# Optimization experiments

Measured on AMD Instinct MI355X. Metric: run time of the kernel, lower is better.

The kernel has to match this reference:

```python
import jax, jax.numpy as jnp
import numpy as np

T = 2048        # document length in tokens
L = 10          # max span width (compute_idx_spans default)
ATTN_DIM = 1024 # states feature dim
EMBED_DIM = 1024
DIST_DIM = 20
HID = 150       # Score hidden_dim default
GI_DIM = 2 * ATTN_DIM + EMBED_DIM + DIST_DIM
BINS = np.array([1, 2, 3, 4, 8, 16, 32, 64])
NEG = -1e10


def _mlp(x, W1, b1, W2, b2, W3, b3):
    # Score module: Linear -> ReLU -> Linear -> ReLU -> Linear (dropout = eval identity)
    h = jax.nn.relu(x @ W1 + b1)
    h = jax.nn.relu(h @ W2 + b2)
    return h @ W3 + b3


def setup_inputs() -> dict:
    key = jax.random.key(0)
    ks = jax.random.split(key, 16)
    s = 0.02
    return {
        "states": jax.random.normal(ks[0], (T, ATTN_DIM), jnp.float32),
        "embeds": jax.random.normal(ks[1], (T, EMBED_DIM), jnp.float32),
        # attention Score (input ATTN_DIM)
        "attn_W1": s * jax.random.normal(ks[2], (ATTN_DIM, HID), jnp.float32),
        "attn_b1": jnp.zeros((HID,), jnp.float32),
        "attn_W2": s * jax.random.normal(ks[3], (HID, HID), jnp.float32),
        "attn_b2": jnp.zeros((HID,), jnp.float32),
        "attn_W3": s * jax.random.normal(ks[4], (HID, 1), jnp.float32),
        "attn_b3": jnp.zeros((1,), jnp.float32),
        # width distance embedding table (len(bins)+1 = 9 rows)
        "width_table": s * jax.random.normal(ks[5], (len(BINS) + 1, DIST_DIM), jnp.float32),
        # mention Score (input GI_DIM)
        "score_W1": s * jax.random.normal(ks[6], (GI_DIM, HID), jnp.float32),
        "score_b1": jnp.zeros((HID,), jnp.float32),
        "score_W2": s * jax.random.normal(ks[7], (HID, HID), jnp.float32),
        "score_b2": jnp.zeros((HID,), jnp.float32),
        "score_W3": s * jax.random.normal(ks[8], (HID, 1), jnp.float32),
        "score_b3": jnp.zeros((1,), jnp.float32),
    }


def reference(states, embeds,
              attn_W1, attn_b1, attn_W2, attn_b2, attn_W3, attn_b3,
              width_table,
              score_W1, score_b1, score_W2, score_b2, score_W3, score_b3):
    # Enumerate all spans with start in [0, T-L] and width 1..L (static shapes).
    starts = jnp.arange(T - L + 1)
    widths = jnp.arange(1, L + 1)
    i1 = jnp.repeat(starts, L)                 # [N]
    w = jnp.tile(widths, T - L + 1)            # [N]
    i2 = i1 + w - 1
    pos = i1[:, None] + jnp.arange(L)[None, :]  # [N, L] (max index T-1)
    mask = jnp.arange(L)[None, :] < w[:, None]  # [N, L]

    # Per-token attention scores, then ragged gather + masked softmax pooling.
    attns = _mlp(states, attn_W1, attn_b1, attn_W2, attn_b2, attn_W3, attn_b3)  # [T, 1]
    span_attns = jnp.where(mask, attns[pos, 0], NEG)        # [N, L] (pad value -1e10)
    attn_weights = jax.nn.softmax(span_attns, axis=1)        # [N, L]
    attn_embeds = jnp.einsum('nl,nle->ne', attn_weights, embeds[pos])  # [N, E]

    # Width bucket embedding: stoi = #bins <= length.
    bin_idx = jnp.searchsorted(jnp.asarray(BINS), w, side='right')
    width_emb = width_table[bin_idx]                         # [N, DIST_DIM]

    start_end = jnp.concatenate([states[i1], states[i2]], axis=1)  # [N, 2*ATTN_DIM]
    g_i = jnp.concatenate([start_end, attn_embeds, width_emb], axis=1)  # [N, GI_DIM]
    mention_scores = _mlp(g_i, score_W1, score_b1, score_W2, score_b2, score_W3, score_b3)  # [N, 1]
    return mention_scores
```

## Files before the change

kernel.cpp:

```cpp
#include <hip/hip_runtime.h>

#define T_TOK 2048
#define AD    1024
#define HID   150
#define LW    10
#define NSTART (T_TOK - LW + 1)
#define NSPAN  (NSTART * LW)
#define RS    152

#define OFF_AH  0
#define OFF_SA  (OFF_AH + T_TOK*RS)
#define OFF_SB  (OFF_SA + T_TOK*RS)
#define OFF_EC  (OFF_SB + T_TOK*RS)
#define OFF_WT  (OFF_EC + T_TOK*RS)
#define OFF_ATT (OFF_WT + 16*RS)
#define OFF_BF16 (OFF_ATT + T_TOK)

typedef __attribute__((ext_vector_type(8))) short bf16x8;
typedef __attribute__((ext_vector_type(4))) float f32x4;

__device__ inline unsigned short f2bf(float f) {
  unsigned u = __builtin_bit_cast(unsigned, f);
  u += 0x7fff + ((u >> 16) & 1);
  return (unsigned short)(u >> 16);
}

__device__ inline unsigned cvt2(float lo, float hi) {
  unsigned r;
  asm("v_cvt_pk_bf16_f32 %0, %1, %2" : "=v"(r) : "v"(lo), "v"(hi));
  return r;
}

__device__ inline void gld16(const void* g, void* l) {
  __builtin_amdgcn_global_load_lds(
      (const __attribute__((address_space(1))) unsigned int*)g,
      (__attribute__((address_space(3))) unsigned int*)l, 16, 0, 0);
}

__global__ __launch_bounds__(256) void k_pack(
    const float* __restrict__ aw1, const float* __restrict__ sw1,
    const float* __restrict__ sw2, const float* __restrict__ aw2,
    const float* __restrict__ width_table, const float* __restrict__ score_b1,
    unsigned short* __restrict__ Wt,
    unsigned short* __restrict__ W2t, unsigned short* __restrict__ AW2t,
    float* __restrict__ ws) {
  __shared__ unsigned short T[152*72];
  const int b = blockIdx.x, t = threadIdx.x;

  if (b < 64) {
    const int grp = b >> 4, kt = b & 15;
    const float* src = (grp == 0) ? aw1 : sw1 + (size_t)(grp-1)*AD*HID;
    const int k0 = kt * 64;
    for (int idx = t; idx < 64*152; idx += 256) {
      int kl = idx / 152, j = idx - kl*152;
      float v = (j < HID) ? src[(size_t)(k0+kl)*HID + j] : 0.f;
      T[j*72 + kl] = f2bf(v);
    }
    __syncthreads();
    for (int u = t; u < 160*8; u += 256) {
      int jj = u >> 3, kc = u & 7;
      bf16x8 v;
      if (jj < 152) v = *(const bf16x8*)&T[jj*72 + kc*8];
      else          v = (bf16x8){0,0,0,0,0,0,0,0};
      *(bf16x8*)&Wt[(size_t)(grp*160 + jj)*AD + k0 + kc*8] = v;
    }
  } else if (b < 264) {
    int idx = (b - 64) * 256 + t;
    const float* src; unsigned short* dst; int u;
    if (idx < 25600) { src = sw2; dst = W2t; u = idx; }
    else             { src = aw2; dst = AW2t; u = idx - 25600; }
    int j = u / 160, k = u - j*160;
    float v = (j < HID && k < HID) ? src[(size_t)k*HID + j] : 0.f;
    dst[u] = f2bf(v);
  } else {
    const int j = t;
    if (j < HID) {
      float* WT = ws + OFF_WT;
      for (int bb = 0; bb < 9; ++bb) {
        float acc = score_b1[j];
#pragma unroll
        for (int d = 0; d < 20; ++d)
          acc = fmaf(width_table[bb*20 + d], sw1[(size_t)(3*AD + d)*HID + j], acc);
        WT[bb*RS + j] = acc;
      }
    }
  }
}

#define BM 32
#define KS 64
__global__ __launch_bounds__(320) void k_gemm(
    const float* __restrict__ st, const float* __restrict__ em,
    const unsigned short* __restrict__ Wt, const float* __restrict__ attn_b1,
    float* __restrict__ ws) {
  const int m0   = blockIdx.x * BM;
  const int s    = blockIdx.y >> 1;
  const int half = blockIdx.y & 1;
  const int tid  = threadIdx.x;
  const int lane = tid & 63, wv = tid >> 6;

  __shared__ unsigned short lA[2][BM*KS];
  __shared__ unsigned short lB[2][80*KS];

  const float* Ag = (s < 3 ? st : em) + (size_t)m0 * AD;
  const unsigned short* Bg = Wt + (size_t)(s*160 + half*80) * AD;

  f32x4 acc0 = {0.f,0.f,0.f,0.f}, acc1 = {0.f,0.f,0.f,0.f};

  auto stageB = [&](int kb, int buf) {
    for (int seg = wv; seg < 10; seg += 5) {
      int c = seg*64 + lane;
      int row = c >> 3, ch = c & 7;
      gld16(Bg + (size_t)row*AD + kb + ((ch ^ (row & 7)) << 3), &lB[buf][seg*512]);
    }
  };
  auto stageA = [&](int kb, int buf) {
    if (tid < 256) {
      int row = tid >> 3, ch = tid & 7;
      const float* src = Ag + (size_t)row*AD + kb + ((ch ^ (row & 7)) << 3);
      float4 a = *(const float4*)src;
      float4 c = *(const float4*)(src + 4);
      uint4 o;
      o.x = cvt2(a.x, a.y); o.y = cvt2(a.z, a.w);
      o.z = cvt2(c.x, c.y); o.w = cvt2(c.z, c.w);
      *(uint4*)&lA[buf][tid*8] = o;
    }
  };

  stageB(0, 0);
  stageA(0, 0);
  int buf = 0;
  const int r = lane & 15, g = lane >> 4;
  const int rx = wv*16 + r;
  const int sw = r & 7;

  for (int kk = 0; kk < 16; ++kk) {
    __syncthreads();
    if (kk < 15) { stageB((kk+1)*KS, buf ^ 1); stageA((kk+1)*KS, buf ^ 1); }
#pragma unroll
    for (int z = 0; z < 2; ++z) {
      const int cz = z*4 + g;
      bf16x8 X  = *(const bf16x8*)&lB[buf][rx*KS      + ((cz ^ sw) << 3)];
      bf16x8 Y0 = *(const bf16x8*)&lA[buf][r*KS       + ((cz ^ sw) << 3)];
      bf16x8 Y1 = *(const bf16x8*)&lA[buf][(16+r)*KS  + ((cz ^ sw) << 3)];
      acc0 = __builtin_amdgcn_mfma_f32_16x16x32_bf16(X, Y0, acc0, 0, 0, 0);
      acc1 = __builtin_amdgcn_mfma_f32_16x16x32_bf16(X, Y1, acc1, 0, 0, 0);
    }
    buf ^= 1;
  }

  const int jn = half*80 + wv*16 + g*4;
  float* Cp = ws + (s==0 ? OFF_AH : s==1 ? OFF_SA : s==2 ? OFF_SB : OFF_EC);
#pragma unroll
  for (int f = 0; f < 2; ++f) {
    int m = m0 + f*16 + r;
    f32x4 a = f ? acc1 : acc0;
    if (s == 0) {
#pragma unroll
      for (int q = 0; q < 4; ++q)
        if (jn + q < HID) a[q] = fmaxf(a[q] + attn_b1[jn+q], 0.f);
    }
    float* d = Cp + (size_t)m*RS + jn;
    if (jn + 3 < HID) *(f32x4*)d = a;
    else {
#pragma unroll
      for (int q = 0; q < 4; ++q) if (jn + q < HID) d[q] = a[q];
    }
  }
}

#define PS 168

#define SPB 8
__global__ __launch_bounds__(640) void k_span(
    const unsigned short* __restrict__ W2t,
    const unsigned short* __restrict__ AW2t,
    const float* __restrict__ ab2, const float* __restrict__ aw3,
    const float* __restrict__ ab3,
    const float* __restrict__ sb2, const float* __restrict__ sw3,
    const float* __restrict__ sb3,
    const float* __restrict__ ws, float* __restrict__ out) {
  const int i1b = blockIdx.x * SPB;
  const int t = threadIdx.x, lane = t & 63, wv = t >> 6;
  const int r = lane & 15, g = lane >> 4;
  __shared__ unsigned short sH[80 * PS];
  __shared__ float red[80][10];
  __shared__ float sATT[32];
  __shared__ float sE[SPB][10], sI[SPB][10];
  const float* AH = ws + OFF_AH;

  for (int u = t; u < 32*160; u += 640) {
    int row = u / 160, jj = u - row*160;
    int tok = i1b + row;
    float v = (row < 17 && jj < HID && tok < T_TOK) ? AH[(size_t)tok*RS + jj] : 0.f;
    sH[row*PS + jj] = f2bf(v);
  }
  __syncthreads();
  {
    const int jt = wv;
    bf16x8 Af[5];
#pragma unroll
    for (int kc = 0; kc < 5; ++kc)
      Af[kc] = *(const bf16x8*)&AW2t[(size_t)(jt*16 + r)*160 + kc*32 + g*8];
    f32x4 acc[2];
#pragma unroll
    for (int nt = 0; nt < 2; ++nt) acc[nt] = (f32x4){0.f,0.f,0.f,0.f};
#pragma unroll
    for (int nt = 0; nt < 2; ++nt)
#pragma unroll
      for (int kc = 0; kc < 5; ++kc) {
        bf16x8 Bf = *(const bf16x8*)&sH[(nt*16 + r)*PS + kc*32 + g*8];
        acc[nt] = __builtin_amdgcn_mfma_f32_16x16x32_bf16(Af[kc], Bf, acc[nt], 0, 0, 0);
      }
    float b2v[4], w3v[4];
#pragma unroll
    for (int q = 0; q < 4; ++q) {
      int j = jt*16 + g*4 + q;
      b2v[q] = (j < HID) ? ab2[j] : 0.f;
      w3v[q] = (j < HID) ? aw3[j] : 0.f;
    }
#pragma unroll
    for (int nt = 0; nt < 2; ++nt) {
      float p = 0.f;
#pragma unroll
      for (int q = 0; q < 4; ++q)
        p += fmaxf(acc[nt][q] + b2v[q], 0.f) * w3v[q];
      p += __shfl_xor(p, 16);
      p += __shfl_xor(p, 32);
      if (g == 0) red[nt*16 + r][wv] = p;
    }
  }
  __syncthreads();
  if (t < 32) {
    float s = ab3[0];
#pragma unroll
    for (int w = 0; w < 10; ++w) s += red[t][w];
    sATT[t] = s;
  }
  __syncthreads();

  if (t < SPB) {
    int i1 = i1b + t;
    if (i1 < NSTART) {
      float a[10];
#pragma unroll
      for (int l = 0; l < 10; ++l) a[l] = sATT[t + l];
      float M = a[0];
#pragma unroll
      for (int l = 1; l < 10; ++l) M = fmaxf(M, a[l]);
      float D = 0.f;
#pragma unroll
      for (int l = 0; l < 10; ++l) {
        float e = expf(a[l] - M);
        D += e;
        sE[t][l] = e;
        sI[t][l] = 1.f / D;
      }
    } else {
#pragma unroll
      for (int l = 0; l < 10; ++l) { sE[t][l] = 0.f; sI[t][l] = 0.f; }
    }
  }
  __syncthreads();

  const float* SA = ws + OFF_SA;
  const float* SBp = ws + OFF_SB;
  const float* EC = ws + OFF_EC;
  const float* WT = ws + OFF_WT;
  const int binrow[10] = {1,2,3,4,4,4,4,5,5,5};

#pragma unroll
  for (int rep = 0; rep < 2; ++rep) {
    int u = rep*640 + t;
    int sl = u / 160, jj = u - sl*160;
    int i1 = i1b + sl;
    if (jj < HID) {
      float sa = SA[(size_t)i1*RS + jj];
      float rs = 0.f;
#pragma unroll
      for (int l = 0; l < 10; ++l) {
        rs = fmaf(sE[sl][l], EC[(size_t)(i1+l)*RS + jj], rs);
        float h = sa + SBp[(size_t)(i1+l)*RS + jj] + WT[binrow[l]*RS + jj]
                + rs * sI[sl][l];
        sH[(sl*10 + l)*PS + jj] = f2bf(fmaxf(h, 0.f));
      }
    } else {
#pragma unroll
      for (int l = 0; l < 10; ++l) sH[(sl*10 + l)*PS + jj] = 0;
    }
  }
  __syncthreads();

  const int jt = wv;
  bf16x8 Af[5];
#pragma unroll
  for (int kc = 0; kc < 5; ++kc)
    Af[kc] = *(const bf16x8*)&W2t[(size_t)(jt*16 + r)*160 + kc*32 + g*8];
  f32x4 acc[5];
#pragma unroll
  for (int nt = 0; nt < 5; ++nt) acc[nt] = (f32x4){0.f,0.f,0.f,0.f};
#pragma unroll
  for (int nt = 0; nt < 5; ++nt)
#pragma unroll
    for (int kc = 0; kc < 5; ++kc) {
      bf16x8 Bf = *(const bf16x8*)&sH[(nt*16 + r)*PS + kc*32 + g*8];
      acc[nt] = __builtin_amdgcn_mfma_f32_16x16x32_bf16(Af[kc], Bf, acc[nt], 0, 0, 0);
    }

  float b2v[4], w3v[4];
#pragma unroll
  for (int q = 0; q < 4; ++q) {
    int j = jt*16 + g*4 + q;
    b2v[q] = (j < HID) ? sb2[j] : 0.f;
    w3v[q] = (j < HID) ? sw3[j] : 0.f;
  }
#pragma unroll
  for (int nt = 0; nt < 5; ++nt) {
    float p = 0.f;
#pragma unroll
    for (int q = 0; q < 4; ++q)
      p += fmaxf(acc[nt][q] + b2v[q], 0.f) * w3v[q];
    p += __shfl_xor(p, 16);
    p += __shfl_xor(p, 32);
    if (g == 0) red[nt*16 + r][wv] = p;
  }
  __syncthreads();
  if (t < 80) {
    int ng = i1b*10 + t;
    if (ng < NSPAN) {
      float s = sb3[0];
#pragma unroll
      for (int w = 0; w < 10; ++w) s += red[t][w];
      out[ng] = s;
    }
  }
}

extern "C" void kernel_launch(void* const* d_in, const int* in_sizes, int n_in,
                              void* d_out, int out_size, void* d_ws, size_t ws_size,
                              hipStream_t stream) {
  const float* states      = (const float*)d_in[0];
  const float* embeds      = (const float*)d_in[1];
  const float* attn_W1     = (const float*)d_in[2];
  const float* attn_b1     = (const float*)d_in[3];
  const float* attn_W2     = (const float*)d_in[4];
  const float* attn_b2     = (const float*)d_in[5];
  const float* attn_W3     = (const float*)d_in[6];
  const float* attn_b3     = (const float*)d_in[7];
  const float* width_table = (const float*)d_in[8];
  const float* score_W1    = (const float*)d_in[9];
  const float* score_b1    = (const float*)d_in[10];
  const float* score_W2    = (const float*)d_in[11];
  const float* score_b2    = (const float*)d_in[12];
  const float* score_W3    = (const float*)d_in[13];
  const float* score_b3    = (const float*)d_in[14];
  float* out = (float*)d_out;
  float* ws  = (float*)d_ws;

  unsigned short* Wt   = (unsigned short*)(ws + OFF_BF16);
  unsigned short* W2t  = Wt + 640*AD;
  unsigned short* AW2t = W2t + 25600;

  k_pack<<<265, 256, 0, stream>>>(attn_W1, score_W1, score_W2, attn_W2,
                                  width_table, score_b1, Wt, W2t, AW2t, ws);
  k_gemm<<<dim3(T_TOK/BM, 8), 320, 0, stream>>>(states, embeds, Wt, attn_b1, ws);
  k_span<<<(NSTART+SPB-1)/SPB, 640, 0, stream>>>(W2t, AW2t,
                                  attn_b2, attn_W3, attn_b3,
                                  score_b2, score_W3, score_b3, ws, out);
}
```

Baseline: 43.09 us.

## Prefetch GEMM A tiles into registers and stage span rows in LDS

```diff
diff --git a/kernel.cpp b/kernel.cpp
--- a/kernel.cpp
+++ b/kernel.cpp
@@ -107,6 +107,9 @@
 
   f32x4 acc0 = {0.f,0.f,0.f,0.f}, acc1 = {0.f,0.f,0.f,0.f};
 
+  const int arow = tid >> 3, ach = tid & 7;
+  const float* asrc = Ag + (size_t)arow*AD + ((ach ^ (arow & 7)) << 3);
+
   auto stageB = [&](int kb, int buf) {
     for (int seg = wv; seg < 10; seg += 5) {
       int c = seg*64 + lane;
@@ -114,29 +117,29 @@
       gld16(Bg + (size_t)row*AD + kb + ((ch ^ (row & 7)) << 3), &lB[buf][seg*512]);
     }
   };
-  auto stageA = [&](int kb, int buf) {
-    if (tid < 256) {
-      int row = tid >> 3, ch = tid & 7;
-      const float* src = Ag + (size_t)row*AD + kb + ((ch ^ (row & 7)) << 3);
-      float4 a = *(const float4*)src;
-      float4 c = *(const float4*)(src + 4);
-      uint4 o;
-      o.x = cvt2(a.x, a.y); o.y = cvt2(a.z, a.w);
-      o.z = cvt2(c.x, c.y); o.w = cvt2(c.z, c.w);
-      *(uint4*)&lA[buf][tid*8] = o;
-    }
-  };
-
-  stageB(0, 0);
-  stageA(0, 0);
-  int buf = 0;
+
   const int r = lane & 15, g = lane >> 4;
   const int rx = wv*16 + r;
   const int sw = r & 7;
 
+  float4 ra, rc;
+  if (tid < 256) { ra = *(const float4*)asrc; rc = *(const float4*)(asrc + 4); }
+  stageB(0, 0);
+  if (tid < 256) {
+    uint4 o;
+    o.x = cvt2(ra.x, ra.y); o.y = cvt2(ra.z, ra.w);
+    o.z = cvt2(rc.x, rc.y); o.w = cvt2(rc.z, rc.w);
+    *(uint4*)&lA[0][tid*8] = o;
+  }
+  __syncthreads();
+
   for (int kk = 0; kk < 16; ++kk) {
-    __syncthreads();
-    if (kk < 15) { stageB((kk+1)*KS, buf ^ 1); stageA((kk+1)*KS, buf ^ 1); }
+    const int buf = kk & 1;
+    if (kk < 15) {
+      const int kb = (kk+1)*KS;
+      if (tid < 256) { ra = *(const float4*)(asrc + kb); rc = *(const float4*)(asrc + kb + 4); }
+      stageB(kb, buf ^ 1);
+    }
 #pragma unroll
     for (int z = 0; z < 2; ++z) {
       const int cz = z*4 + g;
@@ -146,7 +149,13 @@
       acc0 = __builtin_amdgcn_mfma_f32_16x16x32_bf16(X, Y0, acc0, 0, 0, 0);
       acc1 = __builtin_amdgcn_mfma_f32_16x16x32_bf16(X, Y1, acc1, 0, 0, 0);
     }
-    buf ^= 1;
+    if (kk < 15 && tid < 256) {
+      uint4 o;
+      o.x = cvt2(ra.x, ra.y); o.y = cvt2(ra.z, ra.w);
+      o.z = cvt2(rc.x, rc.y); o.w = cvt2(rc.z, rc.w);
+      *(uint4*)&lA[buf ^ 1][tid*8] = o;
+    }
+    __syncthreads();
   }
 
   const int jn = half*80 + wv*16 + g*4;
@@ -170,6 +179,7 @@
 }
 
 #define PS 168
+#define FR 152
 
 #define SPB 8
 __global__ __launch_bounds__(640) void k_span(
@@ -184,10 +194,16 @@
   const int t = threadIdx.x, lane = t & 63, wv = t >> 6;
   const int r = lane & 15, g = lane >> 4;
   __shared__ unsigned short sH[80 * PS];
+  __shared__ float fSB[17*FR], fEC[17*FR];
+  __shared__ float fSA[8*FR],  fWT[6*FR];
   __shared__ float red[80][10];
   __shared__ float sATT[32];
   __shared__ float sE[SPB][10], sI[SPB][10];
-  const float* AH = ws + OFF_AH;
+  const float* AH  = ws + OFF_AH;
+  const float* SA  = ws + OFF_SA;
+  const float* SBp = ws + OFF_SB;
+  const float* EC  = ws + OFF_EC;
+  const float* WT  = ws + OFF_WT;
 
   for (int u = t; u < 32*160; u += 640) {
     int row = u / 160, jj = u - row*160;
@@ -195,7 +211,17 @@
     float v = (row < 17 && jj < HID && tok < T_TOK) ? AH[(size_t)tok*RS + jj] : 0.f;
     sH[row*PS + jj] = f2bf(v);
   }
-  __syncthreads();
+  for (int u = t; u < 48*38; u += 640) {
+    int row = u / 38, c4 = u - row*38;
+    const float* gsrc; float* ldst;
+    if (row < 17)      { gsrc = SBp + (size_t)(i1b+row)*RS;    ldst = fSB + row*FR; }
+    else if (row < 34) { gsrc = EC  + (size_t)(i1b+row-17)*RS; ldst = fEC + (row-17)*FR; }
+    else if (row < 42) { gsrc = SA  + (size_t)(i1b+row-34)*RS; ldst = fSA + (row-34)*FR; }
+    else               { gsrc = WT  + (size_t)(row-42)*RS;     ldst = fWT + (row-42)*FR; }
+    *(float4*)(ldst + c4*4) = *(const float4*)(gsrc + c4*4);
+  }
+  __syncthreads();
+
   {
     const int jt = wv;
     bf16x8 Af[5];
@@ -263,24 +289,18 @@
   }
   __syncthreads();
 
-  const float* SA = ws + OFF_SA;
-  const float* SBp = ws + OFF_SB;
-  const float* EC = ws + OFF_EC;
-  const float* WT = ws + OFF_WT;
   const int binrow[10] = {1,2,3,4,4,4,4,5,5,5};
-
 #pragma unroll
   for (int rep = 0; rep < 2; ++rep) {
     int u = rep*640 + t;
     int sl = u / 160, jj = u - sl*160;
-    int i1 = i1b + sl;
     if (jj < HID) {
-      float sa = SA[(size_t)i1*RS + jj];
+      float sa = fSA[sl*FR + jj];
       float rs = 0.f;
 #pragma unroll
       for (int l = 0; l < 10; ++l) {
-        rs = fmaf(sE[sl][l], EC[(size_t)(i1+l)*RS + jj], rs);
-        float h = sa + SBp[(size_t)(i1+l)*RS + jj] + WT[binrow[l]*RS + jj]
+        rs = fmaf(sE[sl][l], fEC[(sl+l)*FR + jj], rs);
+        float h = sa + fSB[(sl+l)*FR + jj] + fWT[binrow[l]*FR + jj]
                 + rs * sI[sl][l];
         sH[(sl*10 + l)*PS + jj] = f2bf(fmaxf(h, 0.f));
       }
```

After: 43.00 us (median of 2 runs). No clear change (-0.2%).

## Fuse token GEMM into span kernel with per-block LDS token window

Applied to the files above, without the earlier changes.

```diff
diff --git a/kernel.cpp b/kernel.cpp
--- a/kernel.cpp
+++ b/kernel.cpp
@@ -7,14 +7,14 @@
 #define NSTART (T_TOK - LW + 1)
 #define NSPAN  (NSTART * LW)
 #define RS    152
-
-#define OFF_AH  0
-#define OFF_SA  (OFF_AH + T_TOK*RS)
-#define OFF_SB  (OFF_SA + T_TOK*RS)
-#define OFF_EC  (OFF_SB + T_TOK*RS)
-#define OFF_WT  (OFF_EC + T_TOK*RS)
-#define OFF_ATT (OFF_WT + 16*RS)
-#define OFF_BF16 (OFF_ATT + T_TOK)
+#define FR    152
+#define PS    168
+
+#define OFF_WT   0
+#define OFF_BF16 (16*RS)
+
+#define SPB   16
+#define WIN   25
 
 typedef __attribute__((ext_vector_type(8))) short bf16x8;
 typedef __attribute__((ext_vector_type(4))) float f32x4;
@@ -31,17 +31,11 @@
   return r;
 }
 
-__device__ inline void gld16(const void* g, void* l) {
-  __builtin_amdgcn_global_load_lds(
-      (const __attribute__((address_space(1))) unsigned int*)g,
-      (__attribute__((address_space(3))) unsigned int*)l, 16, 0, 0);
-}
-
 __global__ __launch_bounds__(256) void k_pack(
     const float* __restrict__ aw1, const float* __restrict__ sw1,
     const float* __restrict__ sw2, const float* __restrict__ aw2,
     const float* __restrict__ width_table, const float* __restrict__ score_b1,
-    unsigned short* __restrict__ Wt,
+    unsigned short* __restrict__ Wf,
     unsigned short* __restrict__ W2t, unsigned short* __restrict__ AW2t,
     float* __restrict__ ws) {
   __shared__ unsigned short T[152*72];
@@ -62,7 +56,11 @@
       bf16x8 v;
       if (jj < 152) v = *(const bf16x8*)&T[jj*72 + kc*8];
       else          v = (bf16x8){0,0,0,0,0,0,0,0};
-      *(bf16x8*)&Wt[(size_t)(grp*160 + jj)*AD + k0 + kc*8] = v;
+      const int R  = grp*160 + jj;
+      const int nt = R >> 4, r = R & 15;
+      const int k  = k0 + kc*8;
+      const int ks = k >> 5, g = (k >> 3) & 3;
+      *(bf16x8*)&Wf[(size_t)(((nt*32 + ks)*64) + g*16 + r)*8] = v;
     }
   } else if (b < 264) {
     int idx = (b - 64) * 256 + t;
@@ -87,154 +85,184 @@
   }
 }
 
-#define BM 32
-#define KS 64
-__global__ __launch_bounds__(320) void k_gemm(
-    const float* __restrict__ st, const float* __restrict__ em,
-    const unsigned short* __restrict__ Wt, const float* __restrict__ attn_b1,
-    float* __restrict__ ws) {
-  const int m0   = blockIdx.x * BM;
-  const int s    = blockIdx.y >> 1;
-  const int half = blockIdx.y & 1;
-  const int tid  = threadIdx.x;
-  const int lane = tid & 63, wv = tid >> 6;
-
-  __shared__ unsigned short lA[2][BM*KS];
-  __shared__ unsigned short lB[2][80*KS];
-
-  const float* Ag = (s < 3 ? st : em) + (size_t)m0 * AD;
-  const unsigned short* Bg = Wt + (size_t)(s*160 + half*80) * AD;
-
-  f32x4 acc0 = {0.f,0.f,0.f,0.f}, acc1 = {0.f,0.f,0.f,0.f};
-
-  auto stageB = [&](int kb, int buf) {
-    for (int seg = wv; seg < 10; seg += 5) {
-      int c = seg*64 + lane;
-      int row = c >> 3, ch = c & 7;
-      gld16(Bg + (size_t)row*AD + kb + ((ch ^ (row & 7)) << 3), &lB[buf][seg*512]);
-    }
-  };
-  auto stageA = [&](int kb, int buf) {
-    if (tid < 256) {
-      int row = tid >> 3, ch = tid & 7;
-      const float* src = Ag + (size_t)row*AD + kb + ((ch ^ (row & 7)) << 3);
-      float4 a = *(const float4*)src;
-      float4 c = *(const float4*)(src + 4);
-      uint4 o;
-      o.x = cvt2(a.x, a.y); o.y = cvt2(a.z, a.w);
-      o.z = cvt2(c.x, c.y); o.w = cvt2(c.z, c.w);
-      *(uint4*)&lA[buf][tid*8] = o;
-    }
-  };
-
-  stageB(0, 0);
-  stageA(0, 0);
-  int buf = 0;
-  const int r = lane & 15, g = lane >> 4;
-  const int rx = wv*16 + r;
-  const int sw = r & 7;
-
-  for (int kk = 0; kk < 16; ++kk) {
-    __syncthreads();
-    if (kk < 15) { stageB((kk+1)*KS, buf ^ 1); stageA((kk+1)*KS, buf ^ 1); }
-#pragma unroll
-    for (int z = 0; z < 2; ++z) {
-      const int cz = z*4 + g;
-      bf16x8 X  = *(const bf16x8*)&lB[buf][rx*KS      + ((cz ^ sw) << 3)];
-      bf16x8 Y0 = *(const bf16x8*)&lA[buf][r*KS       + ((cz ^ sw) << 3)];
-      bf16x8 Y1 = *(const bf16x8*)&lA[buf][(16+r)*KS  + ((cz ^ sw) << 3)];
-      acc0 = __builtin_amdgcn_mfma_f32_16x16x32_bf16(X, Y0, acc0, 0, 0, 0);
-      acc1 = __builtin_amdgcn_mfma_f32_16x16x32_bf16(X, Y1, acc1, 0, 0, 0);
-    }
-    buf ^= 1;
-  }
-
-  const int jn = half*80 + wv*16 + g*4;
-  float* Cp = ws + (s==0 ? OFF_AH : s==1 ? OFF_SA : s==2 ? OFF_SB : OFF_EC);
-#pragma unroll
-  for (int f = 0; f < 2; ++f) {
-    int m = m0 + f*16 + r;
-    f32x4 a = f ? acc1 : acc0;
-    if (s == 0) {
-#pragma unroll
-      for (int q = 0; q < 4; ++q)
-        if (jn + q < HID) a[q] = fmaxf(a[q] + attn_b1[jn+q], 0.f);
-    }
-    float* d = Cp + (size_t)m*RS + jn;
-    if (jn + 3 < HID) *(f32x4*)d = a;
-    else {
-#pragma unroll
-      for (int q = 0; q < 4; ++q) if (jn + q < HID) d[q] = a[q];
-    }
-  }
-}
-
-#define PS 168
-
-#define SPB 8
-__global__ __launch_bounds__(640) void k_span(
+#define A_OFF   0
+#define AH_OFF  65536
+#define SA_OFF  76288
+#define SB_OFF  95744
+#define EC_OFF  115200
+#define WTL_OFF 134656
+#define RED_OFF 138304
+#define ATT_OFF 144704
+#define E_OFF   144832
+#define I_OFF   145472
+#define LDS_SZ  146112
+
+__global__ __launch_bounds__(640, 1) void k_mega(
+    const unsigned short* __restrict__ Wf,
     const unsigned short* __restrict__ W2t,
     const unsigned short* __restrict__ AW2t,
+    const float* __restrict__ st, const float* __restrict__ em,
+    const float* __restrict__ ab1,
     const float* __restrict__ ab2, const float* __restrict__ aw3,
     const float* __restrict__ ab3,
     const float* __restrict__ sb2, const float* __restrict__ sw3,
     const float* __restrict__ sb3,
     const float* __restrict__ ws, float* __restrict__ out) {
+  __shared__ __align__(16) char L[LDS_SZ];
+  unsigned short* aL  = (unsigned short*)(L + A_OFF);
+  unsigned short* sH2 = (unsigned short*)(L + A_OFF);
+  unsigned short* oAH = (unsigned short*)(L + AH_OFF);
+  float* oSA = (float*)(L + SA_OFF);
+  float* oSB = (float*)(L + SB_OFF);
+  float* oEC = (float*)(L + EC_OFF);
+  float* fWT = (float*)(L + WTL_OFF);
+  float* red = (float*)(L + RED_OFF);
+  float* sATT = (float*)(L + ATT_OFF);
+  float* sE = (float*)(L + E_OFF);
+  float* sI = (float*)(L + I_OFF);
+
   const int i1b = blockIdx.x * SPB;
-  const int t = threadIdx.x, lane = t & 63, wv = t >> 6;
+  const int t = threadIdx.x, lane = t & 63, w = t >> 6;
   const int r = lane & 15, g = lane >> 4;
-  __shared__ unsigned short sH[80 * PS];
-  __shared__ float red[80][10];
-  __shared__ float sATT[32];
-  __shared__ float sE[SPB][10], sI[SPB][10];
-  const float* AH = ws + OFF_AH;
-
-  for (int u = t; u < 32*160; u += 640) {
-    int row = u / 160, jj = u - row*160;
-    int tok = i1b + row;
-    float v = (row < 17 && jj < HID && tok < T_TOK) ? AH[(size_t)tok*RS + jj] : 0.f;
-    sH[row*PS + jj] = f2bf(v);
-  }
-  __syncthreads();
-  {
-    const int jt = wv;
-    bf16x8 Af[5];
-#pragma unroll
-    for (int kc = 0; kc < 5; ++kc)
-      Af[kc] = *(const bf16x8*)&AW2t[(size_t)(jt*16 + r)*160 + kc*32 + g*8];
-    f32x4 acc[2];
-#pragma unroll
-    for (int nt = 0; nt < 2; ++nt) acc[nt] = (f32x4){0.f,0.f,0.f,0.f};
-#pragma unroll
-    for (int nt = 0; nt < 2; ++nt)
-#pragma unroll
-      for (int kc = 0; kc < 5; ++kc) {
-        bf16x8 Bf = *(const bf16x8*)&sH[(nt*16 + r)*PS + kc*32 + g*8];
-        acc[nt] = __builtin_amdgcn_mfma_f32_16x16x32_bf16(Af[kc], Bf, acc[nt], 0, 0, 0);
-      }
+
+  if (t < 6*38) {
+    int row = t / 38, c4 = t - row*38;
+    *(float4*)&fWT[row*FR + c4*4] = *(const float4*)&ws[OFF_WT + row*RS + c4*4];
+  }
+  auto stageA = [&](const float* src) {
+    for (int u = t; u < 32*128; u += 640) {
+      int row = u >> 7, ch = u & 127;
+      int tok = i1b + row;
+      uint4 o;
+      if (row < WIN && tok < T_TOK) {
+        const float* gp = src + (size_t)tok*AD + ch*8;
+        float4 a = *(const float4*)gp, c = *(const float4*)(gp + 4);
+        o.x = cvt2(a.x, a.y); o.y = cvt2(a.z, a.w);
+        o.z = cvt2(c.x, c.y); o.w = cvt2(c.z, c.w);
+      } else o = (uint4){0,0,0,0};
+      *(uint4*)&aL[(size_t)(row*128 + (ch ^ (row & 7)))*8] = o;
+    }
+  };
+  stageA(st);
+  __syncthreads();
+
+  auto ldY = [&](int mt, int ks) {
+    return *(const bf16x8*)&aL[(size_t)(((mt*16 + r)*128) + ((ks*4 + g) ^ (r & 7)))*8];
+  };
+
+  f32x4 a1[3][2];
+#pragma unroll
+  for (int j = 0; j < 3; ++j) { a1[j][0] = (f32x4){0,0,0,0}; a1[j][1] = (f32x4){0,0,0,0}; }
+  {
+    const unsigned short* xp[3];
+#pragma unroll
+    for (int j = 0; j < 3; ++j)
+      xp[j] = Wf + (size_t)(((w + j*10)*32)*64 + lane)*8;
+    bf16x8 X[3], Xn[3];
+#pragma unroll
+    for (int j = 0; j < 3; ++j) X[j] = *(const bf16x8*)xp[j];
+    for (int ks = 0; ks < 32; ++ks) {
+      if (ks < 31) {
+#pragma unroll
+        for (int j = 0; j < 3; ++j) Xn[j] = *(const bf16x8*)(xp[j] + (size_t)(ks+1)*512);
+      }
+      bf16x8 Y0 = ldY(0, ks), Y1 = ldY(1, ks);
+#pragma unroll
+      for (int j = 0; j < 3; ++j) {
+        a1[j][0] = __builtin_amdgcn_mfma_f32_16x16x32_bf16(X[j], Y0, a1[j][0], 0, 0, 0);
+        a1[j][1] = __builtin_amdgcn_mfma_f32_16x16x32_bf16(X[j], Y1, a1[j][1], 0, 0, 0);
+      }
+#pragma unroll
+      for (int j = 0; j < 3; ++j) X[j] = Xn[j];
+    }
+  }
+  __syncthreads();
+  stageA(em);
+  {
+    const int jn = w*16 + g*4;
+#pragma unroll
+    for (int j = 0; j < 3; ++j)
+#pragma unroll
+      for (int mt = 0; mt < 2; ++mt) {
+        f32x4 a = a1[j][mt];
+        const int tokr = mt*16 + r;
+        if (j == 0) {
+#pragma unroll
+          for (int q = 0; q < 4; ++q) {
+            int jj = jn + q;
+            float bb = (jj < HID) ? ab1[jj] : 0.f;
+            oAH[tokr*PS + jj] = f2bf(fmaxf(a[q] + bb, 0.f));
+          }
+        } else {
+          float* dst = (j == 1) ? oSA : oSB;
+#pragma unroll
+          for (int q = 0; q < 4; ++q) {
+            int jj = jn + q;
+            if (jj < FR) dst[tokr*FR + jj] = a[q];
+          }
+        }
+      }
+  }
+  __syncthreads();
+
+  f32x4 a2[2]; a2[0] = (f32x4){0,0,0,0}; a2[1] = (f32x4){0,0,0,0};
+  {
+    const unsigned short* xp2 = Wf + (size_t)(((30 + w)*32)*64 + lane)*8;
+    bf16x8 X2 = *(const bf16x8*)xp2, X2n;
+    for (int ks = 0; ks < 32; ++ks) {
+      if (ks < 31) X2n = *(const bf16x8*)(xp2 + (size_t)(ks+1)*512);
+      bf16x8 Y0 = ldY(0, ks), Y1 = ldY(1, ks);
+      a2[0] = __builtin_amdgcn_mfma_f32_16x16x32_bf16(X2, Y0, a2[0], 0, 0, 0);
+      a2[1] = __builtin_amdgcn_mfma_f32_16x16x32_bf16(X2, Y1, a2[1], 0, 0, 0);
+      X2 = X2n;
+    }
+    const int jn = w*16 + g*4;
+#pragma unroll
+    for (int mt = 0; mt < 2; ++mt) {
+      const int tokr = mt*16 + r;
+#pragma unroll
+      for (int q = 0; q < 4; ++q) {
+        int jj = jn + q;
+        if (jj < FR) oEC[tokr*FR + jj] = a2[mt][q];
+      }
+    }
+  }
+  __syncthreads();
+
+  {
+    f32x4 pa[2]; pa[0] = (f32x4){0,0,0,0}; pa[1] = (f32x4){0,0,0,0};
+#pragma unroll
+    for (int kc = 0; kc < 5; ++kc) {
+      bf16x8 Af = *(const bf16x8*)&AW2t[(size_t)(w*16 + r)*160 + kc*32 + g*8];
+#pragma unroll
+      for (int mt = 0; mt < 2; ++mt) {
+        bf16x8 Yf = *(const bf16x8*)&oAH[(mt*16 + r)*PS + kc*32 + g*8];
+        pa[mt] = __builtin_amdgcn_mfma_f32_16x16x32_bf16(Af, Yf, pa[mt], 0, 0, 0);
+      }
+    }
     float b2v[4], w3v[4];
 #pragma unroll
     for (int q = 0; q < 4; ++q) {
-      int j = jt*16 + g*4 + q;
-      b2v[q] = (j < HID) ? ab2[j] : 0.f;
-      w3v[q] = (j < HID) ? aw3[j] : 0.f;
-    }
-#pragma unroll
-    for (int nt = 0; nt < 2; ++nt) {
+      int jj = w*16 + g*4 + q;
+      b2v[q] = (jj < HID) ? ab2[jj] : 0.f;
+      w3v[q] = (jj < HID) ? aw3[jj] : 0.f;
+    }
+#pragma unroll
+    for (int mt = 0; mt < 2; ++mt) {
       float p = 0.f;
 #pragma unroll
       for (int q = 0; q < 4; ++q)
-        p += fmaxf(acc[nt][q] + b2v[q], 0.f) * w3v[q];
+        p += fmaxf(pa[mt][q] + b2v[q], 0.f) * w3v[q];
       p += __shfl_xor(p, 16);
       p += __shfl_xor(p, 32);
-      if (g == 0) red[nt*16 + r][wv] = p;
+      if (g == 0) red[(mt*16 + r)*10 + w] = p;
     }
   }
   __syncthreads();
   if (t < 32) {
     float s = ab3[0];
 #pragma unroll
-    for (int w = 0; w < 10; ++w) s += red[t][w];
+    for (int q = 0; q < 10; ++q) s += red[t*10 + q];
     sATT[t] = s;
   }
   __syncthreads();
@@ -253,84 +281,78 @@
       for (int l = 0; l < 10; ++l) {
         float e = expf(a[l] - M);
         D += e;
-        sE[t][l] = e;
-        sI[t][l] = 1.f / D;
+        sE[t*10 + l] = e;
+        sI[t*10 + l] = 1.f / D;
       }
     } else {
 #pragma unroll
-      for (int l = 0; l < 10; ++l) { sE[t][l] = 0.f; sI[t][l] = 0.f; }
-    }
-  }
-  __syncthreads();
-
-  const float* SA = ws + OFF_SA;
-  const float* SBp = ws + OFF_SB;
-  const float* EC = ws + OFF_EC;
-  const float* WT = ws + OFF_WT;
+      for (int l = 0; l < 10; ++l) { sE[t*10 + l] = 0.f; sI[t*10 + l] = 0.f; }
+    }
+  }
+  __syncthreads();
+
   const int binrow[10] = {1,2,3,4,4,4,4,5,5,5};
-
-#pragma unroll
-  for (int rep = 0; rep < 2; ++rep) {
+#pragma unroll
+  for (int rep = 0; rep < 4; ++rep) {
     int u = rep*640 + t;
     int sl = u / 160, jj = u - sl*160;
-    int i1 = i1b + sl;
     if (jj < HID) {
-      float sa = SA[(size_t)i1*RS + jj];
+      float sa = oSA[sl*FR + jj];
       float rs = 0.f;
 #pragma unroll
       for (int l = 0; l < 10; ++l) {
-        rs = fmaf(sE[sl][l], EC[(size_t)(i1+l)*RS + jj], rs);
-        float h = sa + SBp[(size_t)(i1+l)*RS + jj] + WT[binrow[l]*RS + jj]
-                + rs * sI[sl][l];
-        sH[(sl*10 + l)*PS + jj] = f2bf(fmaxf(h, 0.f));
+        rs = fmaf(sE[sl*10 + l], oEC[(sl+l)*FR + jj], rs);
+        float h = sa + oSB[(sl+l)*FR + jj] + fWT[binrow[l]*FR + jj]
+                + rs * sI[sl*10 + l];
+        sH2[(sl*10 + l)*PS + jj] = f2bf(fmaxf(h, 0.f));
       }
     } else {
 #pragma unroll
-      for (int l = 0; l < 10; ++l) sH[(sl*10 + l)*PS + jj] = 0;
-    }
-  }
-  __syncthreads();
-
-  const int jt = wv;
-  bf16x8 Af[5];
-#pragma unroll
-  for (int kc = 0; kc < 5; ++kc)
-    Af[kc] = *(const bf16x8*)&W2t[(size_t)(jt*16 + r)*160 + kc*32 + g*8];
-  f32x4 acc[5];
-#pragma unroll
-  for (int nt = 0; nt < 5; ++nt) acc[nt] = (f32x4){0.f,0.f,0.f,0.f};
-#pragma unroll
-  for (int nt = 0; nt < 5; ++nt)
-#pragma unroll
-    for (int kc = 0; kc < 5; ++kc) {
-      bf16x8 Bf = *(const bf16x8*)&sH[(nt*16 + r)*PS + kc*32 + g*8];
-      acc[nt] = __builtin_amdgcn_mfma_f32_16x16x32_bf16(Af[kc], Bf, acc[nt], 0, 0, 0);
-    }
-
-  float b2v[4], w3v[4];
-#pragma unroll
-  for (int q = 0; q < 4; ++q) {
-    int j = jt*16 + g*4 + q;
-    b2v[q] = (j < HID) ? sb2[j] : 0.f;
-    w3v[q] = (j < HID) ? sw3[j] : 0.f;
-  }
-#pragma unroll
-  for (int nt = 0; nt < 5; ++nt) {
-    float p = 0.f;
-#pragma unroll
-    for (int q = 0; q < 4; ++q)
-      p += fmaxf(acc[nt][q] + b2v[q], 0.f) * w3v[q];
-    p += __shfl_xor(p, 16);
-    p += __shfl_xor(p, 32);
-    if (g == 0) red[nt*16 + r][wv] = p;
-  }
-  __syncthreads();
-  if (t < 80) {
+      for (int l = 0; l < 10; ++l) sH2[(sl*10 + l)*PS + jj] = 0;
+    }
+  }
+  __syncthreads();
+
+  {
+    bf16x8 Af[5];
+#pragma unroll
+    for (int kc = 0; kc < 5; ++kc)
+      Af[kc] = *(const bf16x8*)&W2t[(size_t)(w*16 + r)*160 + kc*32 + g*8];
+    f32x4 ac[10];
+#pragma unroll
+    for (int nt = 0; nt < 10; ++nt) ac[nt] = (f32x4){0,0,0,0};
+#pragma unroll
+    for (int nt = 0; nt < 10; ++nt)
+#pragma unroll
+      for (int kc = 0; kc < 5; ++kc) {
+        bf16x8 Bf = *(const bf16x8*)&sH2[(nt*16 + r)*PS + kc*32 + g*8];
+        ac[nt] = __builtin_amdgcn_mfma_f32_16x16x32_bf16(Af[kc], Bf, ac[nt], 0, 0, 0);
+      }
+    float b2v[4], w3v[4];
+#pragma unroll
+    for (int q = 0; q < 4; ++q) {
+      int jj = w*16 + g*4 + q;
+      b2v[q] = (jj < HID) ? sb2[jj] : 0.f;
+      w3v[q] = (jj < HID) ? sw3[jj] : 0.f;
+    }
+#pragma unroll
+    for (int nt = 0; nt < 10; ++nt) {
+      float p = 0.f;
+#pragma unroll
+      for (int q = 0; q < 4; ++q)
+        p += fmaxf(ac[nt][q] + b2v[q], 0.f) * w3v[q];
+      p += __shfl_xor(p, 16);
+      p += __shfl_xor(p, 32);
+      if (g == 0) red[(nt*16 + r)*10 + w] = p;
+    }
+  }
+  __syncthreads();
+  if (t < 160) {
     int ng = i1b*10 + t;
     if (ng < NSPAN) {
       float s = sb3[0];
 #pragma unroll
-      for (int w = 0; w < 10; ++w) s += red[t][w];
+      for (int q = 0; q < 10; ++q) s += red[t*10 + q];
       out[ng] = s;
     }
   }
@@ -357,14 +379,14 @@
   float* out = (float*)d_out;
   float* ws  = (float*)d_ws;
 
-  unsigned short* Wt   = (unsigned short*)(ws + OFF_BF16);
-  unsigned short* W2t  = Wt + 640*AD;
+  unsigned short* Wf   = (unsigned short*)(ws + OFF_BF16);
+  unsigned short* W2t  = Wf + 655360;
   unsigned short* AW2t = W2t + 25600;
 
   k_pack<<<265, 256, 0, stream>>>(attn_W1, score_W1, score_W2, attn_W2,
-                                  width_table, score_b1, Wt, W2t, AW2t, ws);
-  k_gemm<<<dim3(T_TOK/BM, 8), 320, 0, stream>>>(states, embeds, Wt, attn_b1, ws);
-  k_span<<<(NSTART+SPB-1)/SPB, 640, 0, stream>>>(W2t, AW2t,
+                                  width_table, score_b1, Wf, W2t, AW2t, ws);
+  k_mega<<<(NSTART + SPB - 1)/SPB, 640, 0, stream>>>(Wf, W2t, AW2t,
+                                  states, embeds, attn_b1,
                                   attn_b2, attn_W3, attn_b3,
                                   score_b2, score_W3, score_b3, ws, out);
 }
```

Result: slower. 51.06 us (+18.5%).
